# Performance work log

Hardware: AMD Instinct MI355X
Metric: run time of the kernel (lower is better)

## Reference

```python
import jax, jax.numpy as jnp
import numpy as np

D_MODEL = 1024
NUM_HEADS = 16
D_K = D_MODEL // NUM_HEADS
B, S = 4, 2048


def setup_inputs() -> dict:
    key = jax.random.key(0)
    ks = jax.random.split(key, 11)
    s = 1.0 / np.sqrt(D_MODEL)  # torch Linear default init scale (uniform bound)
    def lin(k):
        kw, kb = jax.random.split(k)
        W = jax.random.uniform(kw, (D_MODEL, D_MODEL), jnp.float32, -s, s)
        b = jax.random.uniform(kb, (D_MODEL,), jnp.float32, -s, s)
        return W, b
    Wq, bq = lin(ks[0])
    Wk, bk = lin(ks[1])
    Wv, bv = lin(ks[2])
    Wo, bo = lin(ks[3])
    query = jax.random.normal(ks[4], (B, S, D_MODEL), jnp.float32)
    key_t = jax.random.normal(ks[5], (B, S, D_MODEL), jnp.float32)
    value = jax.random.normal(ks[6], (B, S, D_MODEL), jnp.float32)
    mask = jnp.ones((B, 1, 1, S), jnp.int32)
    return {"query": query, "key": key_t, "value": value, "mask": mask,
            "Wq": Wq, "bq": bq, "Wk": Wk, "bk": bk, "Wv": Wv, "bv": bv,
            "Wo": Wo, "bo": bo}


def _split_heads(x):
    # (B, S, D) -> (B, H, S, d_k)
    b, s, _ = x.shape
    return x.reshape(b, s, NUM_HEADS, D_K).transpose(0, 2, 1, 3)


def _mha(query, key, value, mask, Wq, bq, Wk, bk, Wv, bv, Wo, bo):
    Q = _split_heads(query @ Wq.T + bq)
    K = _split_heads(key @ Wk.T + bk)
    V = _split_heads(value @ Wv.T + bv)
    scores = jnp.einsum('bhqd,bhkd->bhqk', Q, K) / np.sqrt(D_K)
    scores = jnp.where(mask == 0, jnp.float32(-1e9), scores)
    attn = jax.nn.softmax(scores, axis=-1)
    out = jnp.einsum('bhqk,bhkd->bhqd', attn, V)  # (B,H,S,d_k)
    out = out.transpose(0, 2, 1, 3).reshape(out.shape[0], out.shape[2], D_MODEL)
    return out @ Wo.T + bo


def reference(query, key, value, mask, Wq, bq, Wk, bk, Wv, bv, Wo, bo):
    return _mha(query, key, value, mask, Wq, bq, Wk, bk, Wv, bv, Wo, bo)
```

## Files before the change

### kernel.cpp

```cpp
#include <hip/hip_runtime.h>


typedef unsigned short u16;
typedef __attribute__((ext_vector_type(8))) short short8;
typedef __attribute__((ext_vector_type(4))) float f32x4;

__device__ __forceinline__ u16 f2bf(float f) {
  union { float f; unsigned int u; } v; v.f = f;
  return (u16)((v.u + 0x7FFFu + ((v.u >> 16) & 1u)) >> 16);
}

__device__ __forceinline__ void gll16(const void* gptr, void* lptr) {
  __builtin_amdgcn_global_load_lds(
      (const __attribute__((address_space(1))) unsigned int*)gptr,
      (__attribute__((address_space(3))) unsigned int*)lptr, 16, 0, 0);
}

__global__ void cvt_x(const float* __restrict__ s, u16* __restrict__ d, int n) {
  const int i = (blockIdx.x * 256 + threadIdx.x) * 8;
  if (i >= n) return;
  f32x4 a = *(const f32x4*)(s + i);
  f32x4 b = *(const f32x4*)(s + i + 4);
  short8 r;
  r[0] = (short)f2bf(a[0]); r[1] = (short)f2bf(a[1]);
  r[2] = (short)f2bf(a[2]); r[3] = (short)f2bf(a[3]);
  r[4] = (short)f2bf(b[0]); r[5] = (short)f2bf(b[1]);
  r[6] = (short)f2bf(b[2]); r[7] = (short)f2bf(b[3]);
  *(short8*)(d + i) = r;
}

__global__ void cvt_x3(const float* __restrict__ q, const float* __restrict__ k,
                       const float* __restrict__ v, u16* __restrict__ d) {
  const int z = blockIdx.y;
  const float* s = (z == 0) ? q : (z == 1) ? k : v;
  const int i = (blockIdx.x * 256 + threadIdx.x) * 8;
  u16* dz = d + (size_t)z * 8388608;
  f32x4 a = *(const f32x4*)(s + i);
  f32x4 b = *(const f32x4*)(s + i + 4);
  short8 r;
  r[0] = (short)f2bf(a[0]); r[1] = (short)f2bf(a[1]);
  r[2] = (short)f2bf(a[2]); r[3] = (short)f2bf(a[3]);
  r[4] = (short)f2bf(b[0]); r[5] = (short)f2bf(b[1]);
  r[6] = (short)f2bf(b[2]); r[7] = (short)f2bf(b[3]);
  *(short8*)(dz + i) = r;
}

__global__ void cvt_w4(const float* __restrict__ w0, const float* __restrict__ w1,
                       const float* __restrict__ w2, const float* __restrict__ w3,
                       u16* __restrict__ d) {
  const int z = blockIdx.y;
  const float* s = (z == 0) ? w0 : (z == 1) ? w1 : (z == 2) ? w2 : w3;
  const int i = (blockIdx.x * 256 + threadIdx.x) * 8;
  u16* dz = d + (size_t)z * 1048576;
  f32x4 a = *(const f32x4*)(s + i);
  f32x4 b = *(const f32x4*)(s + i + 4);
  short8 r;
  r[0] = (short)f2bf(a[0]); r[1] = (short)f2bf(a[1]);
  r[2] = (short)f2bf(a[2]); r[3] = (short)f2bf(a[3]);
  r[4] = (short)f2bf(b[0]); r[5] = (short)f2bf(b[1]);
  r[6] = (short)f2bf(b[2]); r[7] = (short)f2bf(b[3]);
  *(short8*)(dz + i) = r;
}

__device__ __forceinline__ void xcd_swz(unsigned& bx, unsigned& by) {
  const unsigned nx = gridDim.x, nwg = nx * gridDim.y;
  if ((nwg & 7u) == 0u) {
    const unsigned lin = bx + nx * by;
    const unsigned swz = (lin & 7u) * (nwg >> 3) + (lin >> 3);
    bx = swz % nx;
    by = swz / nx;
  }
}

#define GM 128
#define GN 128
#define GK 32

template <typename TC, bool TRANS>
__global__ __launch_bounds__(256, 3) void gemm_bb(
    const u16* __restrict__ A, const u16* __restrict__ W,
    const float* __restrict__ bias, TC* __restrict__ C,
    int M, int N, int K, float scale)
{
  __shared__ __align__(16) u16 As[2][GM * GK];
  __shared__ __align__(16) u16 Bs[2][GN * GK];

  const int tid  = threadIdx.x;
  const int lane = tid & 63;
  const int l15  = lane & 15;
  const int quad = lane >> 4;
  const int wave = tid >> 6;
  unsigned bxu = blockIdx.x, byu = blockIdx.y;
  xcd_swz(bxu, byu);
  const int bm = byu * GM;
  const int bn = bxu * GN;
  const int wm = (wave >> 1) * 64;
  const int wn = (wave & 1) * 64;

  const f32x4 zero4 = {0.f, 0.f, 0.f, 0.f};
  f32x4 acc[4][4];
#pragma unroll
  for (int i = 0; i < 4; i++)
#pragma unroll
    for (int j = 0; j < 4; j++) acc[i][j] = zero4;

  const int srow = tid >> 2;
  const int chl  = (tid & 3) ^ ((tid >> 3) & 3);
  const u16* Ag = A + (size_t)(bm + srow) * K + chl * 8;
  const u16* Wg = W + (size_t)(bn + srow) * K + chl * 8;
  const size_t rowskip = (size_t)64 * K;
  const int chpA = quad ^ ((l15 >> 1) & 3);

  gll16(Ag, &As[0][tid * 8]);
  gll16(Ag + rowskip, &As[0][tid * 8 + 2048]);
  gll16(Wg, &Bs[0][tid * 8]);
  gll16(Wg + rowskip, &Bs[0][tid * 8 + 2048]);

  int buf = 0;
  for (int k0 = 0; k0 < K; k0 += GK) {
    __syncthreads();
    if (k0 + GK < K) {
      const int nb = buf ^ 1;
      gll16(Ag + k0 + GK, &As[nb][tid * 8]);
      gll16(Ag + k0 + GK + rowskip, &As[nb][tid * 8 + 2048]);
      gll16(Wg + k0 + GK, &Bs[nb][tid * 8]);
      gll16(Wg + k0 + GK + rowskip, &Bs[nb][tid * 8 + 2048]);
    }

    short8 af[4], bfr[4];
#pragma unroll
    for (int mi = 0; mi < 4; mi++)
      af[mi] = *(const short8*)&As[buf][(wm + mi * 16 + l15) * GK + chpA * 8];
#pragma unroll
    for (int ni = 0; ni < 4; ni++)
      bfr[ni] = *(const short8*)&Bs[buf][(wn + ni * 16 + l15) * GK + chpA * 8];
#pragma unroll
    for (int mi = 0; mi < 4; mi++)
#pragma unroll
      for (int ni = 0; ni < 4; ni++)
        acc[mi][ni] = __builtin_amdgcn_mfma_f32_16x16x32_bf16(
            af[mi], bfr[ni], acc[mi][ni], 0, 0, 0);
    buf ^= 1;
  }

  float bval[4];
#pragma unroll
  for (int ni = 0; ni < 4; ni++) bval[ni] = bias[bn + wn + ni * 16 + l15];
#pragma unroll
  for (int mi = 0; mi < 4; mi++) {
    const int m0 = bm + wm + mi * 16 + quad * 4;
#pragma unroll
    for (int ni = 0; ni < 4; ni++) {
      const int n = bn + wn + ni * 16 + l15;
      if constexpr (TRANS) {
        ushort4 w;
        w.x = f2bf((acc[mi][ni][0] + bval[ni]) * scale);
        w.y = f2bf((acc[mi][ni][1] + bval[ni]) * scale);
        w.z = f2bf((acc[mi][ni][2] + bval[ni]) * scale);
        w.w = f2bf((acc[mi][ni][3] + bval[ni]) * scale);
        *(ushort4*)((u16*)C + (size_t)n * M + m0) = w;
      } else {
#pragma unroll
        for (int r = 0; r < 4; r++) {
          const float v = (acc[mi][ni][r] + bval[ni]) * scale;
          if constexpr (sizeof(TC) == 2)
            C[(size_t)(m0 + r) * N + n] = f2bf(v);
          else
            C[(size_t)(m0 + r) * N + n] = v;
        }
      }
    }
  }
}

__global__ __launch_bounds__(256, 3) void gemm_qkv(
    const u16* __restrict__ Ab, const u16* __restrict__ Wc,
    const float* __restrict__ bq, const float* __restrict__ bk,
    const float* __restrict__ bv, u16* __restrict__ Qo,
    u16* __restrict__ Ko, u16* __restrict__ Vo, float qscale)
{
  const int M = 8192, N = 1024, K = 1024;
  const int z = blockIdx.z;
  const u16* A = Ab + (size_t)z * 8388608;
  const u16* W = Wc + (size_t)z * 1048576;
  const float* bias = (z == 0) ? bq : (z == 1) ? bk : bv;
  u16* C = (z == 0) ? Qo : (z == 1) ? Ko : Vo;
  const float scale = (z == 0) ? qscale : 1.0f;
  const bool trans = (z == 2);

  __shared__ __align__(16) u16 As[2][GM * GK];
  __shared__ __align__(16) u16 Bs[2][GN * GK];

  const int tid  = threadIdx.x;
  const int lane = tid & 63;
  const int l15  = lane & 15;
  const int quad = lane >> 4;
  const int wave = tid >> 6;
  unsigned bxu = blockIdx.x, byu = blockIdx.y;
  xcd_swz(bxu, byu);
  const int bm = byu * GM;
  const int bn = bxu * GN;
  const int wm = (wave >> 1) * 64;
  const int wn = (wave & 1) * 64;

  const f32x4 zero4 = {0.f, 0.f, 0.f, 0.f};
  f32x4 acc[4][4];
#pragma unroll
  for (int i = 0; i < 4; i++)
#pragma unroll
    for (int j = 0; j < 4; j++) acc[i][j] = zero4;

  const int srow = tid >> 2;
  const int chl  = (tid & 3) ^ ((tid >> 3) & 3);
  const u16* Ag = A + (size_t)(bm + srow) * K + chl * 8;
  const u16* Wg = W + (size_t)(bn + srow) * K + chl * 8;
  const size_t rowskip = (size_t)64 * K;
  const int chpA = quad ^ ((l15 >> 1) & 3);

  gll16(Ag, &As[0][tid * 8]);
  gll16(Ag + rowskip, &As[0][tid * 8 + 2048]);
  gll16(Wg, &Bs[0][tid * 8]);
  gll16(Wg + rowskip, &Bs[0][tid * 8 + 2048]);

  int buf = 0;
  for (int k0 = 0; k0 < K; k0 += GK) {
    __syncthreads();
    if (k0 + GK < K) {
      const int nb = buf ^ 1;
      gll16(Ag + k0 + GK, &As[nb][tid * 8]);
      gll16(Ag + k0 + GK + rowskip, &As[nb][tid * 8 + 2048]);
      gll16(Wg + k0 + GK, &Bs[nb][tid * 8]);
      gll16(Wg + k0 + GK + rowskip, &Bs[nb][tid * 8 + 2048]);
    }

    short8 af[4], bfr[4];
#pragma unroll
    for (int mi = 0; mi < 4; mi++)
      af[mi] = *(const short8*)&As[buf][(wm + mi * 16 + l15) * GK + chpA * 8];
#pragma unroll
    for (int ni = 0; ni < 4; ni++)
      bfr[ni] = *(const short8*)&Bs[buf][(wn + ni * 16 + l15) * GK + chpA * 8];
#pragma unroll
    for (int mi = 0; mi < 4; mi++)
#pragma unroll
      for (int ni = 0; ni < 4; ni++)
        acc[mi][ni] = __builtin_amdgcn_mfma_f32_16x16x32_bf16(
            af[mi], bfr[ni], acc[mi][ni], 0, 0, 0);
    buf ^= 1;
  }

  float bval[4];
#pragma unroll
  for (int ni = 0; ni < 4; ni++) bval[ni] = bias[bn + wn + ni * 16 + l15];
#pragma unroll
  for (int mi = 0; mi < 4; mi++) {
    const int m0 = bm + wm + mi * 16 + quad * 4;
#pragma unroll
    for (int ni = 0; ni < 4; ni++) {
      const int n = bn + wn + ni * 16 + l15;
      if (trans) {
        ushort4 w;
        w.x = f2bf(acc[mi][ni][0] + bval[ni]);
        w.y = f2bf(acc[mi][ni][1] + bval[ni]);
        w.z = f2bf(acc[mi][ni][2] + bval[ni]);
        w.w = f2bf(acc[mi][ni][3] + bval[ni]);
        *(ushort4*)(C + (size_t)n * M + m0) = w;
      } else {
#pragma unroll
        for (int r = 0; r < 4; r++)
          C[(size_t)(m0 + r) * N + n] = f2bf((acc[mi][ni][r] + bval[ni]) * scale);
      }
    }
  }
}

__global__ __launch_bounds__(256, 4) void attn_fused(
    const u16* __restrict__ Qb, const u16* __restrict__ Kb,
    const u16* __restrict__ VtG, const int* __restrict__ mask,
    u16* __restrict__ Ob)
{
  constexpr int S = 2048, D = 1024;
  __shared__ __align__(16) u16 Ks[64 * 64];
  __shared__ __align__(16) u16 Vs[64 * 64];
  __shared__ __align__(16) u16 Pt[4][32 * 64];

  const int tid  = threadIdx.x;
  const int lane = tid & 63;
  const int wave = tid >> 6;
  const int l15  = lane & 15;
  const int quad = lane >> 4;

  const int lin = blockIdx.x + 16 * blockIdx.y;
  const int swz = (lin & 7) * 128 + (lin >> 3);
  const int b  = swz >> 8;
  const int h  = (swz >> 4) & 15;
  const int qw = (swz & 15) * 128 + wave * 32;

  const u16* Qp = Qb + (size_t)b * S * D + h * 64;
  const u16* Kp = Kb + (size_t)b * S * D + h * 64;
  const u16* Vg = VtG + (size_t)h * 64 * 8192 + b * 2048;
  const int* mp = mask + b * S;

  short8 qf[2][2];
#pragma unroll
  for (int qb = 0; qb < 2; qb++)
#pragma unroll
    for (int c = 0; c < 2; c++)
      qf[qb][c] = *(const short8*)&Qp[(size_t)(qw + qb * 16 + l15) * D + c * 32 + quad * 8];

  const f32x4 zero4 = {0.f, 0.f, 0.f, 0.f};
  f32x4 o_acc[2][4];
#pragma unroll
  for (int qb = 0; qb < 2; qb++)
#pragma unroll
    for (int ni = 0; ni < 4; ni++) o_acc[qb][ni] = zero4;
  f32x4 l_acc[2] = {zero4, zero4};

  const short8 one8 = {(short)0x3f80, (short)0x3f80, (short)0x3f80, (short)0x3f80,
                       (short)0x3f80, (short)0x3f80, (short)0x3f80, (short)0x3f80};

  const int srow = tid >> 3;
  const int chl  = (tid & 7) ^ (srow & 7);
  const int fsw  = l15 & 7;

  unsigned int* tbs = (unsigned int*)&Pt[0][0];
  {
    const int t8 = tid * 8;
    int4 a  = *(const int4*)&mp[t8];
    int4 c4 = *(const int4*)&mp[t8 + 4];
    int ok = ((a.x & a.y & a.z & a.w & c4.x & c4.y & c4.z & c4.w) != 0);
    unsigned long long bb = __ballot(ok);
    if (lane == 0) {
      unsigned int byt = 0;
#pragma unroll
      for (int g = 0; g < 8; g++)
        if (((bb >> (8 * g)) & 0xffull) == 0xffull) byt |= 1u << g;
      tbs[wave] = byt;
    }
  }

#pragma unroll
  for (int p = 0; p < 2; p++)
    gll16(Kp + (size_t)(p * 32 + srow) * D + chl * 8, &Ks[p * 2048 + tid * 8]);

  __syncthreads();
  const unsigned int tilebits = __builtin_amdgcn_readfirstlane(
      tbs[0] | (tbs[1] << 8) | (tbs[2] << 16) | (tbs[3] << 24));

  for (int kt = 0; kt < S; kt += 64) {
    __syncthreads();

#pragma unroll
    for (int p = 0; p < 2; p++)
      gll16(Vg + (size_t)(p * 32 + srow) * 8192 + kt + chl * 8,
            &Vs[p * 2048 + tid * 8]);

    f32x4 sc[2][4];
#pragma unroll
    for (int qb = 0; qb < 2; qb++)
#pragma unroll
      for (int s = 0; s < 4; s++) sc[qb][s] = zero4;
#pragma unroll
    for (int c = 0; c < 2; c++)
#pragma unroll
      for (int s = 0; s < 4; s++) {
        short8 kf = *(const short8*)
            &Ks[(s * 16 + l15) * 64 + ((c * 4 + quad) ^ fsw) * 8];
        sc[0][s] = __builtin_amdgcn_mfma_f32_16x16x32_bf16(kf, qf[0][c], sc[0][s], 0, 0, 0);
        sc[1][s] = __builtin_amdgcn_mfma_f32_16x16x32_bf16(kf, qf[1][c], sc[1][s], 0, 0, 0);
      }

    const bool open = (tilebits >> (kt >> 6)) & 1;
    if (open) {
#pragma unroll
      for (int qb = 0; qb < 2; qb++) {
        const int qrow = qb * 16 + l15;
#pragma unroll
        for (int s = 0; s < 4; s++) {
          unsigned int t[4];
#pragma unroll
          for (int r = 0; r < 4; r++) {
            union { float f; unsigned int u; } pu;
            pu.f = __builtin_amdgcn_exp2f(sc[qb][s][r]);
            t[r] = pu.u;
          }
          uint2 w;
          w.x = __builtin_amdgcn_perm(t[1], t[0], 0x07060302u);
          w.y = __builtin_amdgcn_perm(t[3], t[2], 0x07060302u);
          const int phys = (s * 2 + (quad >> 1)) ^ fsw;
          *(uint2*)&Pt[wave][qrow * 64 + phys * 8 + (quad & 1) * 4] = w;
        }
      }
    } else {
      f32x4 cm[4];
#pragma unroll
      for (int s = 0; s < 4; s++) {
        int4 mv = *(const int4*)&mp[kt + s * 16 + quad * 4];
        cm[s][0] = mv.x ? 0.f : -1.0e9f;
        cm[s][1] = mv.y ? 0.f : -1.0e9f;
        cm[s][2] = mv.z ? 0.f : -1.0e9f;
        cm[s][3] = mv.w ? 0.f : -1.0e9f;
      }
#pragma unroll
      for (int qb = 0; qb < 2; qb++) {
        const int qrow = qb * 16 + l15;
#pragma unroll
        for (int s = 0; s < 4; s++) {
          unsigned int t[4];
#pragma unroll
          for (int r = 0; r < 4; r++) {
            union { float f; unsigned int u; } pu;
            pu.f = __builtin_amdgcn_exp2f(sc[qb][s][r] + cm[s][r]);
            t[r] = pu.u;
          }
          uint2 w;
          w.x = __builtin_amdgcn_perm(t[1], t[0], 0x07060302u);
          w.y = __builtin_amdgcn_perm(t[3], t[2], 0x07060302u);
          const int phys = (s * 2 + (quad >> 1)) ^ fsw;
          *(uint2*)&Pt[wave][qrow * 64 + phys * 8 + (quad & 1) * 4] = w;
        }
      }
    }

    __syncthreads();

    if (kt + 64 < S) {
#pragma unroll
      for (int p = 0; p < 2; p++)
        gll16(Kp + (size_t)(kt + 64 + p * 32 + srow) * D + chl * 8,
              &Ks[p * 2048 + tid * 8]);
    }

#pragma unroll
    for (int c = 0; c < 2; c++) {
      short8 pf[2];
#pragma unroll
      for (int qb = 0; qb < 2; qb++)
        pf[qb] = *(const short8*)
            &Pt[wave][(qb * 16 + l15) * 64 + ((c * 4 + quad) ^ fsw) * 8];
      l_acc[0] = __builtin_amdgcn_mfma_f32_16x16x32_bf16(pf[0], one8, l_acc[0], 0, 0, 0);
      l_acc[1] = __builtin_amdgcn_mfma_f32_16x16x32_bf16(pf[1], one8, l_acc[1], 0, 0, 0);
#pragma unroll
      for (int ni = 0; ni < 4; ni++) {
        short8 vf = *(const short8*)
            &Vs[(ni * 16 + l15) * 64 + ((c * 4 + quad) ^ fsw) * 8];
        o_acc[0][ni] = __builtin_amdgcn_mfma_f32_16x16x32_bf16(pf[0], vf, o_acc[0][ni], 0, 0, 0);
        o_acc[1][ni] = __builtin_amdgcn_mfma_f32_16x16x32_bf16(pf[1], vf, o_acc[1][ni], 0, 0, 0);
      }
    }
  }

  float rl[2][4];
#pragma unroll
  for (int qb = 0; qb < 2; qb++)
#pragma unroll
    for (int r = 0; r < 4; r++) rl[qb][r] = 1.0f / l_acc[qb][r];
#pragma unroll
  for (int qb = 0; qb < 2; qb++) {
    const int q0 = qw + qb * 16 + quad * 4;
#pragma unroll
    for (int ni = 0; ni < 4; ni++)
#pragma unroll
      for (int r = 0; r < 4; r++)
        Ob[(size_t)(b * S + q0 + r) * D + h * 64 + ni * 16 + l15] =
            f2bf(o_acc[qb][ni][r] * rl[qb][r]);
  }
}

extern "C" void kernel_launch(void* const* d_in, const int* in_sizes, int n_in,
                              void* d_out, int out_size, void* d_ws, size_t ws_size,
                              hipStream_t stream) {
  const int M = 8192, N = 1024, K = 1024;
  const float* q    = (const float*)d_in[0];
  const float* k    = (const float*)d_in[1];
  const float* v    = (const float*)d_in[2];
  const int*   mask = (const int*)d_in[3];
  const float* Wq = (const float*)d_in[4];
  const float* bq = (const float*)d_in[5];
  const float* Wk = (const float*)d_in[6];
  const float* bk = (const float*)d_in[7];
  const float* Wv = (const float*)d_in[8];
  const float* bv = (const float*)d_in[9];
  const float* Wo = (const float*)d_in[10];
  const float* bo = (const float*)d_in[11];

  const size_t MN = (size_t)M * N;
  const float QSC = 0.125f * 1.44269504f;

  dim3 bb(256);
  dim3 gg(N / GN, M / GM);

  const size_t need_batched = (6 * MN + 4 * 1048576) * sizeof(u16);
  if (ws_size >= need_batched) {
    u16* Ax  = (u16*)d_ws;
    u16* Qb  = Ax + 3 * MN;
    u16* Kb  = Ax + 4 * MN;
    u16* VtG = Ax + 5 * MN;
    u16* Wc  = Ax + 6 * MN;
    u16* Ob  = Ax;

    cvt_w4<<<dim3(512, 4), bb, 0, stream>>>(Wq, Wk, Wv, Wo, Wc);
    cvt_x3<<<dim3(4096, 3), bb, 0, stream>>>(q, k, v, Ax);
    gemm_qkv<<<dim3(8, 64, 3), bb, 0, stream>>>(Ax, Wc, bq, bk, bv, Qb, Kb, VtG, QSC);
    attn_fused<<<dim3(16, 64), bb, 0, stream>>>(Qb, Kb, VtG, mask, Ob);
    gemm_bb<float, false><<<gg, bb, 0, stream>>>(Ob, Wc + 3 * 1048576, bo,
                                                 (float*)d_out, M, N, K, 1.0f);
  } else {
    u16* Qb  = (u16*)d_ws;
    u16* Kb  = Qb + MN;
    u16* VtG = Kb + MN;
    u16* Ob  = VtG + MN;
    u16* Wc  = Ob + MN;
    const int xblk = (int)(MN / (256 * 8));

    cvt_w4<<<dim3(512, 4), bb, 0, stream>>>(Wq, Wk, Wv, Wo, Wc);

    cvt_x<<<xblk, bb, 0, stream>>>(q, Ob, M * N);
    gemm_bb<u16, false><<<gg, bb, 0, stream>>>(Ob, Wc + 0 * 1048576, bq, Qb, M, N, K, QSC);
    cvt_x<<<xblk, bb, 0, stream>>>(k, Ob, M * N);
    gemm_bb<u16, false><<<gg, bb, 0, stream>>>(Ob, Wc + 1 * 1048576, bk, Kb, M, N, K, 1.0f);
    cvt_x<<<xblk, bb, 0, stream>>>(v, Ob, M * N);
    gemm_bb<u16, true><<<gg, bb, 0, stream>>>(Ob, Wc + 2 * 1048576, bv, VtG, M, N, K, 1.0f);

    attn_fused<<<dim3(16, 64), bb, 0, stream>>>(Qb, Kb, VtG, mask, Ob);

    gemm_bb<float, false><<<gg, bb, 0, stream>>>(Ob, Wc + 3 * 1048576, bo,
                                                 (float*)d_out, M, N, K, 1.0f);
  }
}
```

Before: 334.5 us.

## Fuse fp32-to-bf16 input conversion into QKV GEMM and raise MFMA wave priority

After: 352.4 us. 1.05x slower.

```diff
diff --git a/kernel.cpp b/kernel.cpp
--- a/kernel.cpp
+++ b/kernel.cpp
@@ -16,33 +16,13 @@
       (__attribute__((address_space(3))) unsigned int*)lptr, 16, 0, 0);
 }
 
-__global__ void cvt_x(const float* __restrict__ s, u16* __restrict__ d, int n) {
-  const int i = (blockIdx.x * 256 + threadIdx.x) * 8;
-  if (i >= n) return;
-  f32x4 a = *(const f32x4*)(s + i);
-  f32x4 b = *(const f32x4*)(s + i + 4);
+__device__ __forceinline__ void cvt_store8(u16* lds, f32x4 a, f32x4 b) {
   short8 r;
   r[0] = (short)f2bf(a[0]); r[1] = (short)f2bf(a[1]);
   r[2] = (short)f2bf(a[2]); r[3] = (short)f2bf(a[3]);
   r[4] = (short)f2bf(b[0]); r[5] = (short)f2bf(b[1]);
   r[6] = (short)f2bf(b[2]); r[7] = (short)f2bf(b[3]);
-  *(short8*)(d + i) = r;
-}
-
-__global__ void cvt_x3(const float* __restrict__ q, const float* __restrict__ k,
-                       const float* __restrict__ v, u16* __restrict__ d) {
-  const int z = blockIdx.y;
-  const float* s = (z == 0) ? q : (z == 1) ? k : v;
-  const int i = (blockIdx.x * 256 + threadIdx.x) * 8;
-  u16* dz = d + (size_t)z * 8388608;
-  f32x4 a = *(const f32x4*)(s + i);
-  f32x4 b = *(const f32x4*)(s + i + 4);
-  short8 r;
-  r[0] = (short)f2bf(a[0]); r[1] = (short)f2bf(a[1]);
-  r[2] = (short)f2bf(a[2]); r[3] = (short)f2bf(a[3]);
-  r[4] = (short)f2bf(b[0]); r[5] = (short)f2bf(b[1]);
-  r[6] = (short)f2bf(b[2]); r[7] = (short)f2bf(b[3]);
-  *(short8*)(dz + i) = r;
+  *(short8*)lds = r;
 }
 
 __global__ void cvt_w4(const float* __restrict__ w0, const float* __restrict__ w1,
@@ -174,14 +154,15 @@
 }
 
 __global__ __launch_bounds__(256, 3) void gemm_qkv(
-    const u16* __restrict__ Ab, const u16* __restrict__ Wc,
+    const float* __restrict__ qf, const float* __restrict__ kf,
+    const float* __restrict__ vf, const u16* __restrict__ Wc,
     const float* __restrict__ bq, const float* __restrict__ bk,
     const float* __restrict__ bv, u16* __restrict__ Qo,
     u16* __restrict__ Ko, u16* __restrict__ Vo, float qscale)
 {
   const int M = 8192, N = 1024, K = 1024;
   const int z = blockIdx.z;
-  const u16* A = Ab + (size_t)z * 8388608;
+  const float* A = (z == 0) ? qf : (z == 1) ? kf : vf;
   const u16* W = Wc + (size_t)z * 1048576;
   const float* bias = (z == 0) ? bq : (z == 1) ? bk : bv;
   u16* C = (z == 0) ? Qo : (z == 1) ? Ko : Vo;
@@ -212,23 +193,34 @@
 
   const int srow = tid >> 2;
   const int chl  = (tid & 3) ^ ((tid >> 3) & 3);
-  const u16* Ag = A + (size_t)(bm + srow) * K + chl * 8;
+  const float* Af = A + (size_t)(bm + srow) * K + chl * 8;
   const u16* Wg = W + (size_t)(bn + srow) * K + chl * 8;
-  const size_t rowskip = (size_t)64 * K;
+  const size_t rowskip  = (size_t)64 * K;
   const int chpA = quad ^ ((l15 >> 1) & 3);
 
-  gll16(Ag, &As[0][tid * 8]);
-  gll16(Ag + rowskip, &As[0][tid * 8 + 2048]);
+  {
+    f32x4 a0 = *(const f32x4*)(Af);
+    f32x4 a1 = *(const f32x4*)(Af + 4);
+    f32x4 a2 = *(const f32x4*)(Af + rowskip);
+    f32x4 a3 = *(const f32x4*)(Af + rowskip + 4);
+    cvt_store8(&As[0][tid * 8], a0, a1);
+    cvt_store8(&As[0][tid * 8 + 2048], a2, a3);
+  }
   gll16(Wg, &Bs[0][tid * 8]);
   gll16(Wg + rowskip, &Bs[0][tid * 8 + 2048]);
 
   int buf = 0;
   for (int k0 = 0; k0 < K; k0 += GK) {
     __syncthreads();
-    if (k0 + GK < K) {
+    const bool more = (k0 + GK < K);
+    f32x4 a0, a1, a2, a3;
+    if (more) {
       const int nb = buf ^ 1;
-      gll16(Ag + k0 + GK, &As[nb][tid * 8]);
-      gll16(Ag + k0 + GK + rowskip, &As[nb][tid * 8 + 2048]);
+      const float* Ap = Af + k0 + GK;
+      a0 = *(const f32x4*)(Ap);
+      a1 = *(const f32x4*)(Ap + 4);
+      a2 = *(const f32x4*)(Ap + rowskip);
+      a3 = *(const f32x4*)(Ap + rowskip + 4);
       gll16(Wg + k0 + GK, &Bs[nb][tid * 8]);
       gll16(Wg + k0 + GK + rowskip, &Bs[nb][tid * 8 + 2048]);
     }
@@ -246,6 +238,12 @@
       for (int ni = 0; ni < 4; ni++)
         acc[mi][ni] = __builtin_amdgcn_mfma_f32_16x16x32_bf16(
             af[mi], bfr[ni], acc[mi][ni], 0, 0, 0);
+
+    if (more) {
+      const int nb = buf ^ 1;
+      cvt_store8(&As[nb][tid * 8], a0, a1);
+      cvt_store8(&As[nb][tid * 8 + 2048], a2, a3);
+    }
     buf ^= 1;
   }
 
@@ -360,6 +358,7 @@
     for (int qb = 0; qb < 2; qb++)
 #pragma unroll
       for (int s = 0; s < 4; s++) sc[qb][s] = zero4;
+    __builtin_amdgcn_s_setprio(1);
 #pragma unroll
     for (int c = 0; c < 2; c++)
 #pragma unroll
@@ -369,6 +368,7 @@
         sc[0][s] = __builtin_amdgcn_mfma_f32_16x16x32_bf16(kf, qf[0][c], sc[0][s], 0, 0, 0);
         sc[1][s] = __builtin_amdgcn_mfma_f32_16x16x32_bf16(kf, qf[1][c], sc[1][s], 0, 0, 0);
       }
+    __builtin_amdgcn_s_setprio(0);
 
     const bool open = (tilebits >> (kt >> 6)) & 1;
     if (open) {
@@ -431,6 +431,7 @@
               &Ks[p * 2048 + tid * 8]);
     }
 
+    __builtin_amdgcn_s_setprio(1);
 #pragma unroll
     for (int c = 0; c < 2; c++) {
       short8 pf[2];
@@ -448,6 +449,7 @@
         o_acc[1][ni] = __builtin_amdgcn_mfma_f32_16x16x32_bf16(pf[1], vf, o_acc[1][ni], 0, 0, 0);
       }
     }
+    __builtin_amdgcn_s_setprio(0);
   }
 
   float rl[2][4];
@@ -490,41 +492,16 @@
   dim3 bb(256);
   dim3 gg(N / GN, M / GM);
 
-  const size_t need_batched = (6 * MN + 4 * 1048576) * sizeof(u16);
-  if (ws_size >= need_batched) {
-    u16* Ax  = (u16*)d_ws;
-    u16* Qb  = Ax + 3 * MN;
-    u16* Kb  = Ax + 4 * MN;
-    u16* VtG = Ax + 5 * MN;
-    u16* Wc  = Ax + 6 * MN;
-    u16* Ob  = Ax;
-
-    cvt_w4<<<dim3(512, 4), bb, 0, stream>>>(Wq, Wk, Wv, Wo, Wc);
-    cvt_x3<<<dim3(4096, 3), bb, 0, stream>>>(q, k, v, Ax);
-    gemm_qkv<<<dim3(8, 64, 3), bb, 0, stream>>>(Ax, Wc, bq, bk, bv, Qb, Kb, VtG, QSC);
-    attn_fused<<<dim3(16, 64), bb, 0, stream>>>(Qb, Kb, VtG, mask, Ob);
-    gemm_bb<float, false><<<gg, bb, 0, stream>>>(Ob, Wc + 3 * 1048576, bo,
-                                                 (float*)d_out, M, N, K, 1.0f);
-  } else {
-    u16* Qb  = (u16*)d_ws;
-    u16* Kb  = Qb + MN;
-    u16* VtG = Kb + MN;
-    u16* Ob  = VtG + MN;
-    u16* Wc  = Ob + MN;
-    const int xblk = (int)(MN / (256 * 8));
-
-    cvt_w4<<<dim3(512, 4), bb, 0, stream>>>(Wq, Wk, Wv, Wo, Wc);
-
-    cvt_x<<<xblk, bb, 0, stream>>>(q, Ob, M * N);
-    gemm_bb<u16, false><<<gg, bb, 0, stream>>>(Ob, Wc + 0 * 1048576, bq, Qb, M, N, K, QSC);
-    cvt_x<<<xblk, bb, 0, stream>>>(k, Ob, M * N);
-    gemm_bb<u16, false><<<gg, bb, 0, stream>>>(Ob, Wc + 1 * 1048576, bk, Kb, M, N, K, 1.0f);
-    cvt_x<<<xblk, bb, 0, stream>>>(v, Ob, M * N);
-    gemm_bb<u16, true><<<gg, bb, 0, stream>>>(Ob, Wc + 2 * 1048576, bv, VtG, M, N, K, 1.0f);
-
-    attn_fused<<<dim3(16, 64), bb, 0, stream>>>(Qb, Kb, VtG, mask, Ob);
-
-    gemm_bb<float, false><<<gg, bb, 0, stream>>>(Ob, Wc + 3 * 1048576, bo,
-                                                 (float*)d_out, M, N, K, 1.0f);
-  }
-}
+  u16* Qb  = (u16*)d_ws;
+  u16* Kb  = Qb + MN;
+  u16* VtG = Kb + MN;
+  u16* Ob  = VtG + MN;
+  u16* Wc  = Ob + MN;
+
+  cvt_w4<<<dim3(512, 4), bb, 0, stream>>>(Wq, Wk, Wv, Wo, Wc);
+  gemm_qkv<<<dim3(8, 64, 3), bb, 0, stream>>>(q, k, v, Wc, bq, bk, bv,
+                                              Qb, Kb, VtG, QSC);
+  attn_fused<<<dim3(16, 64), bb, 0, stream>>>(Qb, Kb, VtG, mask, Ob);
+  gemm_bb<float, false><<<gg, bb, 0, stream>>>(Ob, Wc + 3 * 1048576, bo,
+                                               (float*)d_out, M, N, K, 1.0f);
+}
```
